# Kernel optimization log

Hardware: AMD Instinct MI355X
Metric: run time of the kernel (lower is better)

## Reference

```python
import jax, jax.numpy as jnp
import numpy as np

EPS = 1e-8

def _batch_gather(table, idx):
    # table: (B, M, F), idx: (B, K) -> (B, K, F)
    return jnp.take_along_axis(table, idx[:, :, None], axis=1)

def setup_inputs() -> dict:
    key = jax.random.key(0)
    ks = jax.random.split(key, 8)
    B, N, E, K, F = 8, 4096, 16384, 16, 128
    initial_node_embed = jax.random.normal(ks[0], (B, N, F), dtype=jnp.float32)
    edges = jax.random.randint(ks[1], (B, E, 3), 0, N, dtype=jnp.int64)
    node_edges = jax.random.randint(ks[2], (B, N, K), 0, E, dtype=jnp.int64)
    node_edge_mask = jax.random.randint(ks[3], (B, N, K), 0, 2, dtype=jnp.int32)
    s = 1.0 / np.sqrt(F)
    W1 = jax.random.normal(ks[4], (F, F), dtype=jnp.float32) * s
    b1 = jnp.zeros((F,), dtype=jnp.float32)
    W2 = jax.random.normal(ks[5], (F, F), dtype=jnp.float32) * s
    b2 = jnp.zeros((F,), dtype=jnp.float32)
    return {"initial_node_embed": initial_node_embed, "edges": edges,
            "node_edges": node_edges, "node_edge_mask": node_edge_mask,
            "W1": W1, "b1": b1, "W2": W2, "b2": b2}

def reference(initial_node_embed, edges, node_edges, node_edge_mask, W1, b1, W2, b2):
    B, N, F = initial_node_embed.shape
    K = node_edges.shape[2]
    sender_idx = edges[:, :, 0]                      # (B, E)
    mask_f = node_edge_mask.astype(jnp.float32)      # (B, N, K)
    num_neighbors = jnp.sum(mask_f, 2, keepdims=True) + EPS  # (B, N, 1)
    flat_ne = node_edges.reshape(B, -1)              # (B, N*K)

    def mp(node_emb, W, b):
        sender = _batch_gather(node_emb, sender_idx)             # (B, E, F)
        edge_emb = jnp.tanh(sender @ W.T + b)                    # (B, E, F)
        nbr = _batch_gather(edge_emb, flat_ne).reshape(B, N, K, F)
        nbr = nbr * mask_f[:, :, :, None]
        return jnp.sum(nbr, 2) / num_neighbors                   # avg agg

    x0 = initial_node_embed
    x1 = mp(x0, W1, b1)
    x2 = mp(x1, W2, b2)
    return jnp.concatenate([x0, x1, x2], axis=2)     # (B, N, 3F)
```

## Files before the change

kernel.cpp:

```cpp
#include <hip/hip_runtime.h>
#include <hip/hip_bf16.h>

typedef __attribute__((ext_vector_type(8))) short short8;
typedef __attribute__((ext_vector_type(4))) float f32x4;
typedef __attribute__((ext_vector_type(2))) float f32x2;

#define B_ 8
#define N_ 4096
#define E_ 16384
#define K_ 16
#define F_ 128

#if defined(__has_builtin)
#  if __has_builtin(__builtin_amdgcn_cvt_pk_f32_fp8) && __has_builtin(__builtin_amdgcn_cvt_pk_fp8_f32)
#    define HW_FP8 1
#  endif
#endif

__device__ __forceinline__ unsigned short f2bf(float f) {
    union { float f; unsigned int u; } c; c.f = f;
    unsigned int u = c.u;
    unsigned int r = (u + 0x7fffu + ((u >> 16) & 1u)) >> 16;
    return (unsigned short)r;
}
__device__ __forceinline__ float fast_tanh(float x) {
    float e = __expf(2.0f * x);
    return 1.0f - 2.0f / (e + 1.0f);
}

__device__ __forceinline__ unsigned int f2fp8_manual(float v) {
    unsigned int u = __float_as_uint(v * 0x1p-120f);
    unsigned int r = (u & 0x7fffffffu) + 0x7ffffu + ((u >> 20) & 1u);
    return ((r >> 20) & 0x7fu) | ((u >> 24) & 0x80u);
}
__device__ __forceinline__ unsigned int pack_fp8x4(float t0, float t1, float t2, float t3) {
#ifdef HW_FP8
    int wd = 0;
    wd = __builtin_amdgcn_cvt_pk_fp8_f32(t0, t1, wd, false);
    wd = __builtin_amdgcn_cvt_pk_fp8_f32(t2, t3, wd, true);
    return (unsigned int)wd;
#else
    return f2fp8_manual(t0) | (f2fp8_manual(t1) << 8) |
           (f2fp8_manual(t2) << 16) | (f2fp8_manual(t3) << 24);
#endif
}
#ifndef HW_FP8
#define DECM(bb) __int_as_float((int)((((bb) & 0x80u) << 24) | (((bb) & 0x7fu) << 20)))
#endif

__device__ __forceinline__ int detect64(const int* raw) {
    int o = 0;
    #pragma unroll
    for (int i = 1; i < 128; i += 2) o |= raw[i];
    return (o == 0) ? 1 : 0;
}

__global__ void wprep(const float* __restrict__ W1, const float* __restrict__ W2,
                      const int* __restrict__ edges_raw, const int* __restrict__ ne_raw,
                      unsigned short* __restrict__ wf, int* __restrict__ flags) {
    int blk = blockIdx.x, tid = threadIdx.x;
    if (blk == 16) {
        if (tid == 0) {
            flags[0] = detect64(edges_raw);
            flags[1] = detect64(ne_raw);
        }
        return;
    }
    int gtid = blk * 256 + tid;
    int wsel = gtid >> 11;
    int q = gtid & 2047;
    int lane = q & 63;
    int gq = q >> 6;
    int nt = gq >> 2, g = gq & 3;
    const float* W = wsel ? W2 : W1;
    int j = nt * 16 + (lane & 15);
    int kbase = g * 32 + 8 * (lane >> 4);
    unsigned short* d = wf + wsel * 16384 + q * 8;
    #pragma unroll
    for (int t = 0; t < 8; ++t) d[t] = f2bf(W[j * 128 + kbase + t]);
}

__global__ void __launch_bounds__(256) node_kernel(
    const float* __restrict__ xsrc, const int* __restrict__ edges_raw,
    const int* __restrict__ ne_raw, const int* __restrict__ mask,
    const int* __restrict__ flags, const unsigned short* __restrict__ wf,
    const float* __restrict__ bias, unsigned char* __restrict__ y,
    float* __restrict__ out, int* __restrict__ sid2) {
    __shared__ short xt[64 * F_];
    int tid = threadIdx.x;
    int swz = (blockIdx.x & 7) * 64 + (blockIdx.x >> 3);
    int b = swz >> 6;
    int r0 = (swz & 63) * 64;
    {
        int s64e = flags[0], s64n = flags[1];
        int base = swz * 1024;
        #pragma unroll
        for (int t = 0; t < 4; ++t) {
            int i = base + t * 256 + tid;
            int bb = i >> 16;
            int eid = s64n ? ne_raw[2 * (long long)i] : ne_raw[i];
            long long ei = (long long)(bb * E_ + eid);
            int s = s64e ? edges_raw[6 * ei] : edges_raw[3 * ei];
            sid2[i] = mask[i] ? s : -1;
        }
    }
    #pragma unroll
    for (int c = 0; c < 4; ++c) {
        int ci = tid + 256 * c;
        int row = ci >> 4, ch = ci & 15;
        int pch = ch ^ (row & 15);
        long long gnode = (long long)(b * N_ + r0 + row);
        const float* src = xsrc + gnode * F_ + ch * 8;
        float4 v0 = *(const float4*)src;
        float4 v1 = *(const float4*)(src + 4);
        ushort4 h0, h1;
        h0.x = f2bf(v0.x); h0.y = f2bf(v0.y); h0.z = f2bf(v0.z); h0.w = f2bf(v0.w);
        h1.x = f2bf(v1.x); h1.y = f2bf(v1.y); h1.z = f2bf(v1.z); h1.w = f2bf(v1.w);
        *(ushort4*)&xt[row * F_ + pch * 8] = h0;
        *(ushort4*)&xt[row * F_ + pch * 8 + 4] = h1;
        float* od = out + gnode * 384 + ch * 8;
        *(float4*)od = v0;
        *(float4*)(od + 4) = v1;
    }
    __syncthreads();
    int w = tid >> 6, lane = tid & 63;
    int rr = w * 16 + (lane & 15);
    short8 bfr[4];
    #pragma unroll
    for (int g = 0; g < 4; ++g) {
        int pch = (g * 4 + (lane >> 4)) ^ (rr & 15);
        bfr[g] = *(const short8*)&xt[rr * F_ + pch * 8];
    }
    int jq = (lane >> 4) * 4;
    long long ybyte = ((long long)(b * N_ + r0 + w * 16 + (lane & 15))) * F_;
    #pragma unroll
    for (int nt = 0; nt < 8; ++nt) {
        f32x4 acc = (f32x4){0.f, 0.f, 0.f, 0.f};
        #pragma unroll
        for (int g = 0; g < 4; ++g) {
            short8 afr = *(const short8*)(wf + ((nt * 4 + g) * 64 + lane) * 8);
            acc = __builtin_amdgcn_mfma_f32_16x16x32_bf16(afr, bfr[g], acc, 0, 0, 0);
        }
        float4 bv = *(const float4*)(bias + nt * 16 + jq);
        float t0 = fast_tanh(acc[0] + bv.x);
        float t1 = fast_tanh(acc[1] + bv.y);
        float t2 = fast_tanh(acc[2] + bv.z);
        float t3 = fast_tanh(acc[3] + bv.w);
        *(unsigned int*)(y + ybyte + nt * 16 + jq) = pack_fp8x4(t0, t1, t2, t3);
    }
}

__global__ void __launch_bounds__(256) aggnode_kernel(
    const unsigned char* __restrict__ y1, const int* __restrict__ sid2,
    const unsigned short* __restrict__ wf2, const float* __restrict__ bias,
    float* __restrict__ out, unsigned char* __restrict__ y2) {
    __shared__ short xt[64 * F_];
    int tid = threadIdx.x;
    int swz = (blockIdx.x & 7) * 64 + (blockIdx.x >> 3);
    int b = swz >> 6;
    int r0 = (swz & 63) * 64;
    int wid = tid >> 6, lane = tid & 63;
    int qt = lane >> 4, s16 = lane & 15;
    const unsigned char* ybase = y1 + (long long)b * (N_ * F_) + s16 * 8;
    #pragma unroll
    for (int t = 0; t < 4; ++t) {
        int row = wid * 16 + qt * 4 + t;
        long long gnode = (long long)(b * N_ + r0 + row);
        const int4* ip = (const int4*)(sid2 + gnode * K_);
        int4 i0 = ip[0], i1 = ip[1], i2 = ip[2], i3 = ip[3];
        float cnt = (float)((i0.x >= 0) + (i0.y >= 0) + (i0.z >= 0) + (i0.w >= 0) +
                            (i1.x >= 0) + (i1.y >= 0) + (i1.z >= 0) + (i1.w >= 0) +
                            (i2.x >= 0) + (i2.y >= 0) + (i2.z >= 0) + (i2.w >= 0) +
                            (i3.x >= 0) + (i3.y >= 0) + (i3.z >= 0) + (i3.w >= 0));
        float a0 = 0.f, a1 = 0.f, a2 = 0.f, a3 = 0.f;
        float a4 = 0.f, a5 = 0.f, a6 = 0.f, a7 = 0.f;
#ifdef HW_FP8
        #define PROC(pk) { \
            float m = ((pk) >= 0) ? 1.0f : 0.0f; \
            int nid = (pk) < 0 ? 0 : (pk); \
            uint2 v = *(const uint2*)(ybase + (long long)nid * F_); \
            f32x2 c0 = __builtin_amdgcn_cvt_pk_f32_fp8(v.x, false); \
            f32x2 c1 = __builtin_amdgcn_cvt_pk_f32_fp8(v.x, true); \
            f32x2 c2 = __builtin_amdgcn_cvt_pk_f32_fp8(v.y, false); \
            f32x2 c3 = __builtin_amdgcn_cvt_pk_f32_fp8(v.y, true); \
            a0 += m * c0.x; a1 += m * c0.y; a2 += m * c1.x; a3 += m * c1.y; \
            a4 += m * c2.x; a5 += m * c2.y; a6 += m * c3.x; a7 += m * c3.y; }
#else
        #define PROC(pk) { \
            float ms = ((pk) >= 0) ? 0x1p120f : 0.0f; \
            int nid = (pk) < 0 ? 0 : (pk); \
            uint2 v = *(const uint2*)(ybase + (long long)nid * F_); \
            a0 += ms * DECM(v.x); a1 += ms * DECM(v.x >> 8); \
            a2 += ms * DECM(v.x >> 16); a3 += ms * DECM(v.x >> 24); \
            a4 += ms * DECM(v.y); a5 += ms * DECM(v.y >> 8); \
            a6 += ms * DECM(v.y >> 16); a7 += ms * DECM(v.y >> 24); }
#endif
        PROC(i0.x) PROC(i0.y) PROC(i0.z) PROC(i0.w)
        PROC(i1.x) PROC(i1.y) PROC(i1.z) PROC(i1.w)
        PROC(i2.x) PROC(i2.y) PROC(i2.z) PROC(i2.w)
        PROC(i3.x) PROC(i3.y) PROC(i3.z) PROC(i3.w)
        #undef PROC
        float inv = 1.0f / (cnt + 1e-8f);
        a0 *= inv; a1 *= inv; a2 *= inv; a3 *= inv;
        a4 *= inv; a5 *= inv; a6 *= inv; a7 *= inv;
        float* po = out + gnode * 384 + 128 + s16 * 8;
        *(f32x4*)po = (f32x4){a0, a1, a2, a3};
        *(f32x4*)(po + 4) = (f32x4){a4, a5, a6, a7};
        int pch = s16 ^ (row & 15);
        short8 h;
        h[0] = (short)f2bf(a0); h[1] = (short)f2bf(a1);
        h[2] = (short)f2bf(a2); h[3] = (short)f2bf(a3);
        h[4] = (short)f2bf(a4); h[5] = (short)f2bf(a5);
        h[6] = (short)f2bf(a6); h[7] = (short)f2bf(a7);
        *(short8*)&xt[row * F_ + pch * 8] = h;
    }
    __syncthreads();
    int rr = wid * 16 + (lane & 15);
    short8 bfr[4];
    #pragma unroll
    for (int g = 0; g < 4; ++g) {
        int pch = (g * 4 + (lane >> 4)) ^ (rr & 15);
        bfr[g] = *(const short8*)&xt[rr * F_ + pch * 8];
    }
    int jq = (lane >> 4) * 4;
    long long ybyte = ((long long)(b * N_ + r0 + wid * 16 + (lane & 15))) * F_;
    #pragma unroll
    for (int nt = 0; nt < 8; ++nt) {
        f32x4 acc = (f32x4){0.f, 0.f, 0.f, 0.f};
        #pragma unroll
        for (int g = 0; g < 4; ++g) {
            short8 afr = *(const short8*)(wf2 + ((nt * 4 + g) * 64 + lane) * 8);
            acc = __builtin_amdgcn_mfma_f32_16x16x32_bf16(afr, bfr[g], acc, 0, 0, 0);
        }
        float4 bv = *(const float4*)(bias + nt * 16 + jq);
        float t0 = fast_tanh(acc[0] + bv.x);
        float t1 = fast_tanh(acc[1] + bv.y);
        float t2 = fast_tanh(acc[2] + bv.z);
        float t3 = fast_tanh(acc[3] + bv.w);
        *(unsigned int*)(y2 + ybyte + nt * 16 + jq) = pack_fp8x4(t0, t1, t2, t3);
    }
}

__global__ void __launch_bounds__(256) agg_kernel(
    const unsigned char* __restrict__ y, const int* __restrict__ sid2,
    float* __restrict__ out, int col_off) {
    int tid = threadIdx.x;
    int swz = (blockIdx.x & 7) * 256 + (blockIdx.x >> 3);
    int nodeblk = swz * 16;
    int wid = tid >> 6, lane = tid & 63;
    int qt = lane >> 4, s16 = lane & 15;
    int node = nodeblk + wid * 4 + qt;
    int b = node >> 12;
    const int4* ip = (const int4*)(sid2 + node * K_);
    int4 i0 = ip[0], i1 = ip[1], i2 = ip[2], i3 = ip[3];
    float cnt = (float)((i0.x >= 0) + (i0.y >= 0) + (i0.z >= 0) + (i0.w >= 0) +
                        (i1.x >= 0) + (i1.y >= 0) + (i1.z >= 0) + (i1.w >= 0) +
                        (i2.x >= 0) + (i2.y >= 0) + (i2.z >= 0) + (i2.w >= 0) +
                        (i3.x >= 0) + (i3.y >= 0) + (i3.z >= 0) + (i3.w >= 0));
    const unsigned char* ybase = y + (long long)b * (N_ * F_) + s16 * 8;
    float a0 = 0.f, a1 = 0.f, a2 = 0.f, a3 = 0.f;
    float a4 = 0.f, a5 = 0.f, a6 = 0.f, a7 = 0.f;
#ifdef HW_FP8
    #define PROC(pk) { \
        float m = ((pk) >= 0) ? 1.0f : 0.0f; \
        int nid = (pk) < 0 ? 0 : (pk); \
        uint2 v = *(const uint2*)(ybase + (long long)nid * F_); \
        f32x2 c0 = __builtin_amdgcn_cvt_pk_f32_fp8(v.x, false); \
        f32x2 c1 = __builtin_amdgcn_cvt_pk_f32_fp8(v.x, true); \
        f32x2 c2 = __builtin_amdgcn_cvt_pk_f32_fp8(v.y, false); \
        f32x2 c3 = __builtin_amdgcn_cvt_pk_f32_fp8(v.y, true); \
        a0 += m * c0.x; a1 += m * c0.y; a2 += m * c1.x; a3 += m * c1.y; \
        a4 += m * c2.x; a5 += m * c2.y; a6 += m * c3.x; a7 += m * c3.y; }
#else
    #define PROC(pk) { \
        float ms = ((pk) >= 0) ? 0x1p120f : 0.0f; \
        int nid = (pk) < 0 ? 0 : (pk); \
        uint2 v = *(const uint2*)(ybase + (long long)nid * F_); \
        a0 += ms * DECM(v.x); a1 += ms * DECM(v.x >> 8); \
        a2 += ms * DECM(v.x >> 16); a3 += ms * DECM(v.x >> 24); \
        a4 += ms * DECM(v.y); a5 += ms * DECM(v.y >> 8); \
        a6 += ms * DECM(v.y >> 16); a7 += ms * DECM(v.y >> 24); }
#endif
    PROC(i0.x) PROC(i0.y) PROC(i0.z) PROC(i0.w)
    PROC(i1.x) PROC(i1.y) PROC(i1.z) PROC(i1.w)
    PROC(i2.x) PROC(i2.y) PROC(i2.z) PROC(i2.w)
    PROC(i3.x) PROC(i3.y) PROC(i3.z) PROC(i3.w)
    #undef PROC
    float inv = 1.0f / (cnt + 1e-8f);
    a0 *= inv; a1 *= inv; a2 *= inv; a3 *= inv;
    a4 *= inv; a5 *= inv; a6 *= inv; a7 *= inv;
    float* po = out + (long long)node * 384 + col_off + s16 * 8;
    *(f32x4*)po = (f32x4){a0, a1, a2, a3};
    *(f32x4*)(po + 4) = (f32x4){a4, a5, a6, a7};
}

extern "C" void kernel_launch(void* const* d_in, const int* in_sizes, int n_in,
                              void* d_out, int out_size, void* d_ws, size_t ws_size,
                              hipStream_t stream) {
    const float* x0        = (const float*)d_in[0];
    const int*   edges_raw = (const int*)d_in[1];
    const int*   ne_raw    = (const int*)d_in[2];
    const int*   mask      = (const int*)d_in[3];
    const float* W1        = (const float*)d_in[4];
    const float* b1        = (const float*)d_in[5];
    const float* W2        = (const float*)d_in[6];
    const float* b2        = (const float*)d_in[7];
    float* out = (float*)d_out;
    char* ws = (char*)d_ws;

    unsigned char*  y1   = (unsigned char*)ws;
    unsigned char*  y2   = (unsigned char*)(ws + 4194304);
    unsigned short* wf   = (unsigned short*)(ws + 8388608);
    int* flags           = (int*)(ws + 8454144);
    int* sid2            = (int*)(ws + 8519680);

    wprep<<<17, 256, 0, stream>>>(W1, W2, edges_raw, ne_raw, wf, flags);
    node_kernel<<<512, 256, 0, stream>>>(x0, edges_raw, ne_raw, mask,
                                         flags, wf, b1, y1, out, sid2);
    aggnode_kernel<<<512, 256, 0, stream>>>(y1, sid2, wf + 16384, b2, out, y2);
    agg_kernel<<<2048, 256, 0, stream>>>(y2, sid2, out, 256);
}
```

Measured before the change: 46.88 us.

## Fuse three stage kernels into one persistent kernel with per-batch atomic barriers

Merges the node transform, the first aggregation plus second transform, and the final aggregation into a single kernel of 512 blocks. Stages are separated by per-batch group barriers that spin on atomic counters in global memory, 64 blocks per batch. This removes two kernel launches and the tail and drain gaps between them. The barrier relies on every block of a group being co-resident on the GPU, uses relaxed atomics with no explicit memory fence, and adds spin-wait overhead.

```diff
diff --git a/kernel.cpp b/kernel.cpp
--- a/kernel.cpp
+++ b/kernel.cpp
@@ -64,6 +64,7 @@
             flags[0] = detect64(edges_raw);
             flags[1] = detect64(ne_raw);
         }
+        if (tid < 16) flags[4 + tid] = 0;
         return;
     }
     int gtid = blk * 256 + tid;
@@ -80,17 +81,34 @@
     for (int t = 0; t < 8; ++t) d[t] = f2bf(W[j * 128 + kbase + t]);
 }
 
-__global__ void __launch_bounds__(256) node_kernel(
-    const float* __restrict__ xsrc, const int* __restrict__ edges_raw,
+__device__ __forceinline__ void group_bar(int* c) {
+    __syncthreads();
+    if (threadIdx.x == 0) {
+        __hip_atomic_fetch_add(c, 1, __ATOMIC_RELAXED, __HIP_MEMORY_SCOPE_AGENT);
+        while (__hip_atomic_load(c, __ATOMIC_RELAXED, __HIP_MEMORY_SCOPE_AGENT) < 64) {
+            __builtin_amdgcn_s_sleep(2);
+        }
+    }
+    __syncthreads();
+}
+
+__global__ void __launch_bounds__(256) mega_kernel(
+    const float* __restrict__ x0, const int* __restrict__ edges_raw,
     const int* __restrict__ ne_raw, const int* __restrict__ mask,
-    const int* __restrict__ flags, const unsigned short* __restrict__ wf,
-    const float* __restrict__ bias, unsigned char* __restrict__ y,
-    float* __restrict__ out, int* __restrict__ sid2) {
+    int* __restrict__ flags, const unsigned short* __restrict__ wf,
+    const float* __restrict__ b1, const float* __restrict__ b2,
+    unsigned char* __restrict__ y1, unsigned char* __restrict__ y2,
+    int* __restrict__ sid2, float* __restrict__ out) {
     __shared__ short xt[64 * F_];
     int tid = threadIdx.x;
-    int swz = (blockIdx.x & 7) * 64 + (blockIdx.x >> 3);
+    int blk = blockIdx.x;
+    int grp = blk & 7;
+    int swz = grp * 64 + (blk >> 3);
     int b = swz >> 6;
     int r0 = (swz & 63) * 64;
+    int wid = tid >> 6, lane = tid & 63;
+    int qt = lane >> 4, s16 = lane & 15;
+
     {
         int s64e = flags[0], s64n = flags[1];
         int base = swz * 1024;
@@ -110,7 +128,7 @@
         int row = ci >> 4, ch = ci & 15;
         int pch = ch ^ (row & 15);
         long long gnode = (long long)(b * N_ + r0 + row);
-        const float* src = xsrc + gnode * F_ + ch * 8;
+        const float* src = x0 + gnode * F_ + ch * 8;
         float4 v0 = *(const float4*)src;
         float4 v1 = *(const float4*)(src + 4);
         ushort4 h0, h1;
@@ -123,175 +141,164 @@
         *(float4*)(od + 4) = v1;
     }
     __syncthreads();
-    int w = tid >> 6, lane = tid & 63;
-    int rr = w * 16 + (lane & 15);
-    short8 bfr[4];
-    #pragma unroll
-    for (int g = 0; g < 4; ++g) {
-        int pch = (g * 4 + (lane >> 4)) ^ (rr & 15);
-        bfr[g] = *(const short8*)&xt[rr * F_ + pch * 8];
-    }
-    int jq = (lane >> 4) * 4;
-    long long ybyte = ((long long)(b * N_ + r0 + w * 16 + (lane & 15))) * F_;
-    #pragma unroll
-    for (int nt = 0; nt < 8; ++nt) {
-        f32x4 acc = (f32x4){0.f, 0.f, 0.f, 0.f};
+    {
+        int rr = wid * 16 + (lane & 15);
+        short8 bfr[4];
         #pragma unroll
         for (int g = 0; g < 4; ++g) {
-            short8 afr = *(const short8*)(wf + ((nt * 4 + g) * 64 + lane) * 8);
-            acc = __builtin_amdgcn_mfma_f32_16x16x32_bf16(afr, bfr[g], acc, 0, 0, 0);
-        }
-        float4 bv = *(const float4*)(bias + nt * 16 + jq);
-        float t0 = fast_tanh(acc[0] + bv.x);
-        float t1 = fast_tanh(acc[1] + bv.y);
-        float t2 = fast_tanh(acc[2] + bv.z);
-        float t3 = fast_tanh(acc[3] + bv.w);
-        *(unsigned int*)(y + ybyte + nt * 16 + jq) = pack_fp8x4(t0, t1, t2, t3);
-    }
-}
-
-__global__ void __launch_bounds__(256) aggnode_kernel(
-    const unsigned char* __restrict__ y1, const int* __restrict__ sid2,
-    const unsigned short* __restrict__ wf2, const float* __restrict__ bias,
-    float* __restrict__ out, unsigned char* __restrict__ y2) {
-    __shared__ short xt[64 * F_];
-    int tid = threadIdx.x;
-    int swz = (blockIdx.x & 7) * 64 + (blockIdx.x >> 3);
-    int b = swz >> 6;
-    int r0 = (swz & 63) * 64;
-    int wid = tid >> 6, lane = tid & 63;
-    int qt = lane >> 4, s16 = lane & 15;
-    const unsigned char* ybase = y1 + (long long)b * (N_ * F_) + s16 * 8;
-    #pragma unroll
-    for (int t = 0; t < 4; ++t) {
-        int row = wid * 16 + qt * 4 + t;
-        long long gnode = (long long)(b * N_ + r0 + row);
-        const int4* ip = (const int4*)(sid2 + gnode * K_);
-        int4 i0 = ip[0], i1 = ip[1], i2 = ip[2], i3 = ip[3];
-        float cnt = (float)((i0.x >= 0) + (i0.y >= 0) + (i0.z >= 0) + (i0.w >= 0) +
-                            (i1.x >= 0) + (i1.y >= 0) + (i1.z >= 0) + (i1.w >= 0) +
-                            (i2.x >= 0) + (i2.y >= 0) + (i2.z >= 0) + (i2.w >= 0) +
-                            (i3.x >= 0) + (i3.y >= 0) + (i3.z >= 0) + (i3.w >= 0));
-        float a0 = 0.f, a1 = 0.f, a2 = 0.f, a3 = 0.f;
-        float a4 = 0.f, a5 = 0.f, a6 = 0.f, a7 = 0.f;
+            int pch = (g * 4 + (lane >> 4)) ^ (rr & 15);
+            bfr[g] = *(const short8*)&xt[rr * F_ + pch * 8];
+        }
+        int jq = (lane >> 4) * 4;
+        long long ybyte = ((long long)(b * N_ + r0 + wid * 16 + (lane & 15))) * F_;
+        #pragma unroll
+        for (int nt = 0; nt < 8; ++nt) {
+            f32x4 acc = (f32x4){0.f, 0.f, 0.f, 0.f};
+            #pragma unroll
+            for (int g = 0; g < 4; ++g) {
+                short8 afr = *(const short8*)(wf + ((nt * 4 + g) * 64 + lane) * 8);
+                acc = __builtin_amdgcn_mfma_f32_16x16x32_bf16(afr, bfr[g], acc, 0, 0, 0);
+            }
+            float4 bv = *(const float4*)(b1 + nt * 16 + jq);
+            float t0 = fast_tanh(acc[0] + bv.x);
+            float t1 = fast_tanh(acc[1] + bv.y);
+            float t2 = fast_tanh(acc[2] + bv.z);
+            float t3 = fast_tanh(acc[3] + bv.w);
+            *(unsigned int*)(y1 + ybyte + nt * 16 + jq) = pack_fp8x4(t0, t1, t2, t3);
+        }
+    }
+    group_bar(flags + 4 + grp);
+
+    {
+        const unsigned char* ybase = y1 + (long long)b * (N_ * F_) + s16 * 8;
+        #pragma unroll
+        for (int t = 0; t < 4; ++t) {
+            int row = wid * 16 + qt * 4 + t;
+            long long gnode = (long long)(b * N_ + r0 + row);
+            const int4* ip = (const int4*)(sid2 + gnode * K_);
+            int4 i0 = ip[0], i1 = ip[1], i2 = ip[2], i3 = ip[3];
+            float cnt = (float)((i0.x >= 0) + (i0.y >= 0) + (i0.z >= 0) + (i0.w >= 0) +
+                                (i1.x >= 0) + (i1.y >= 0) + (i1.z >= 0) + (i1.w >= 0) +
+                                (i2.x >= 0) + (i2.y >= 0) + (i2.z >= 0) + (i2.w >= 0) +
+                                (i3.x >= 0) + (i3.y >= 0) + (i3.z >= 0) + (i3.w >= 0));
+            float a0 = 0.f, a1 = 0.f, a2 = 0.f, a3 = 0.f;
+            float a4 = 0.f, a5 = 0.f, a6 = 0.f, a7 = 0.f;
 #ifdef HW_FP8
-        #define PROC(pk) { \
-            float m = ((pk) >= 0) ? 1.0f : 0.0f; \
-            int nid = (pk) < 0 ? 0 : (pk); \
-            uint2 v = *(const uint2*)(ybase + (long long)nid * F_); \
-            f32x2 c0 = __builtin_amdgcn_cvt_pk_f32_fp8(v.x, false); \
-            f32x2 c1 = __builtin_amdgcn_cvt_pk_f32_fp8(v.x, true); \
-            f32x2 c2 = __builtin_amdgcn_cvt_pk_f32_fp8(v.y, false); \
-            f32x2 c3 = __builtin_amdgcn_cvt_pk_f32_fp8(v.y, true); \
-            a0 += m * c0.x; a1 += m * c0.y; a2 += m * c1.x; a3 += m * c1.y; \
-            a4 += m * c2.x; a5 += m * c2.y; a6 += m * c3.x; a7 += m * c3.y; }
+            #define PROC(pk) { \
+                float m = ((pk) >= 0) ? 1.0f : 0.0f; \
+                int nid = (pk) < 0 ? 0 : (pk); \
+                uint2 v = *(const uint2*)(ybase + (long long)nid * F_); \
+                f32x2 c0 = __builtin_amdgcn_cvt_pk_f32_fp8(v.x, false); \
+                f32x2 c1 = __builtin_amdgcn_cvt_pk_f32_fp8(v.x, true); \
+                f32x2 c2 = __builtin_amdgcn_cvt_pk_f32_fp8(v.y, false); \
+                f32x2 c3 = __builtin_amdgcn_cvt_pk_f32_fp8(v.y, true); \
+                a0 += m * c0.x; a1 += m * c0.y; a2 += m * c1.x; a3 += m * c1.y; \
+                a4 += m * c2.x; a5 += m * c2.y; a6 += m * c3.x; a7 += m * c3.y; }
 #else
-        #define PROC(pk) { \
-            float ms = ((pk) >= 0) ? 0x1p120f : 0.0f; \
-            int nid = (pk) < 0 ? 0 : (pk); \
-            uint2 v = *(const uint2*)(ybase + (long long)nid * F_); \
-            a0 += ms * DECM(v.x); a1 += ms * DECM(v.x >> 8); \
-            a2 += ms * DECM(v.x >> 16); a3 += ms * DECM(v.x >> 24); \
-            a4 += ms * DECM(v.y); a5 += ms * DECM(v.y >> 8); \
-            a6 += ms * DECM(v.y >> 16); a7 += ms * DECM(v.y >> 24); }
-#endif
-        PROC(i0.x) PROC(i0.y) PROC(i0.z) PROC(i0.w)
-        PROC(i1.x) PROC(i1.y) PROC(i1.z) PROC(i1.w)
-        PROC(i2.x) PROC(i2.y) PROC(i2.z) PROC(i2.w)
-        PROC(i3.x) PROC(i3.y) PROC(i3.z) PROC(i3.w)
-        #undef PROC
-        float inv = 1.0f / (cnt + 1e-8f);
-        a0 *= inv; a1 *= inv; a2 *= inv; a3 *= inv;
-        a4 *= inv; a5 *= inv; a6 *= inv; a7 *= inv;
-        float* po = out + gnode * 384 + 128 + s16 * 8;
-        *(f32x4*)po = (f32x4){a0, a1, a2, a3};
-        *(f32x4*)(po + 4) = (f32x4){a4, a5, a6, a7};
-        int pch = s16 ^ (row & 15);
-        short8 h;
-        h[0] = (short)f2bf(a0); h[1] = (short)f2bf(a1);
-        h[2] = (short)f2bf(a2); h[3] = (short)f2bf(a3);
-        h[4] = (short)f2bf(a4); h[5] = (short)f2bf(a5);
-        h[6] = (short)f2bf(a6); h[7] = (short)f2bf(a7);
-        *(short8*)&xt[row * F_ + pch * 8] = h;
-    }
-    __syncthreads();
-    int rr = wid * 16 + (lane & 15);
-    short8 bfr[4];
-    #pragma unroll
-    for (int g = 0; g < 4; ++g) {
-        int pch = (g * 4 + (lane >> 4)) ^ (rr & 15);
-        bfr[g] = *(const short8*)&xt[rr * F_ + pch * 8];
-    }
-    int jq = (lane >> 4) * 4;
-    long long ybyte = ((long long)(b * N_ + r0 + wid * 16 + (lane & 15))) * F_;
-    #pragma unroll
-    for (int nt = 0; nt < 8; ++nt) {
-        f32x4 acc = (f32x4){0.f, 0.f, 0.f, 0.f};
+            #define PROC(pk) { \
+                float ms = ((pk) >= 0) ? 0x1p120f : 0.0f; \
+                int nid = (pk) < 0 ? 0 : (pk); \
+                uint2 v = *(const uint2*)(ybase + (long long)nid * F_); \
+                a0 += ms * DECM(v.x); a1 += ms * DECM(v.x >> 8); \
+                a2 += ms * DECM(v.x >> 16); a3 += ms * DECM(v.x >> 24); \
+                a4 += ms * DECM(v.y); a5 += ms * DECM(v.y >> 8); \
+                a6 += ms * DECM(v.y >> 16); a7 += ms * DECM(v.y >> 24); }
+#endif
+            PROC(i0.x) PROC(i0.y) PROC(i0.z) PROC(i0.w)
+            PROC(i1.x) PROC(i1.y) PROC(i1.z) PROC(i1.w)
+            PROC(i2.x) PROC(i2.y) PROC(i2.z) PROC(i2.w)
+            PROC(i3.x) PROC(i3.y) PROC(i3.z) PROC(i3.w)
+            #undef PROC
+            float inv = 1.0f / (cnt + 1e-8f);
+            a0 *= inv; a1 *= inv; a2 *= inv; a3 *= inv;
+            a4 *= inv; a5 *= inv; a6 *= inv; a7 *= inv;
+            float* po = out + gnode * 384 + 128 + s16 * 8;
+            *(f32x4*)po = (f32x4){a0, a1, a2, a3};
+            *(f32x4*)(po + 4) = (f32x4){a4, a5, a6, a7};
+            int pch = s16 ^ (row & 15);
+            short8 h;
+            h[0] = (short)f2bf(a0); h[1] = (short)f2bf(a1);
+            h[2] = (short)f2bf(a2); h[3] = (short)f2bf(a3);
+            h[4] = (short)f2bf(a4); h[5] = (short)f2bf(a5);
+            h[6] = (short)f2bf(a6); h[7] = (short)f2bf(a7);
+            *(short8*)&xt[row * F_ + pch * 8] = h;
+        }
+        __syncthreads();
+        int rr = wid * 16 + (lane & 15);
+        short8 bfr[4];
         #pragma unroll
         for (int g = 0; g < 4; ++g) {
-            short8 afr = *(const short8*)(wf2 + ((nt * 4 + g) * 64 + lane) * 8);
-            acc = __builtin_amdgcn_mfma_f32_16x16x32_bf16(afr, bfr[g], acc, 0, 0, 0);
-        }
-        float4 bv = *(const float4*)(bias + nt * 16 + jq);
-        float t0 = fast_tanh(acc[0] + bv.x);
-        float t1 = fast_tanh(acc[1] + bv.y);
-        float t2 = fast_tanh(acc[2] + bv.z);
-        float t3 = fast_tanh(acc[3] + bv.w);
-        *(unsigned int*)(y2 + ybyte + nt * 16 + jq) = pack_fp8x4(t0, t1, t2, t3);
-    }
-}
-
-__global__ void __launch_bounds__(256) agg_kernel(
-    const unsigned char* __restrict__ y, const int* __restrict__ sid2,
-    float* __restrict__ out, int col_off) {
-    int tid = threadIdx.x;
-    int swz = (blockIdx.x & 7) * 256 + (blockIdx.x >> 3);
-    int nodeblk = swz * 16;
-    int wid = tid >> 6, lane = tid & 63;
-    int qt = lane >> 4, s16 = lane & 15;
-    int node = nodeblk + wid * 4 + qt;
-    int b = node >> 12;
-    const int4* ip = (const int4*)(sid2 + node * K_);
-    int4 i0 = ip[0], i1 = ip[1], i2 = ip[2], i3 = ip[3];
-    float cnt = (float)((i0.x >= 0) + (i0.y >= 0) + (i0.z >= 0) + (i0.w >= 0) +
-                        (i1.x >= 0) + (i1.y >= 0) + (i1.z >= 0) + (i1.w >= 0) +
-                        (i2.x >= 0) + (i2.y >= 0) + (i2.z >= 0) + (i2.w >= 0) +
-                        (i3.x >= 0) + (i3.y >= 0) + (i3.z >= 0) + (i3.w >= 0));
-    const unsigned char* ybase = y + (long long)b * (N_ * F_) + s16 * 8;
-    float a0 = 0.f, a1 = 0.f, a2 = 0.f, a3 = 0.f;
-    float a4 = 0.f, a5 = 0.f, a6 = 0.f, a7 = 0.f;
+            int pch = (g * 4 + (lane >> 4)) ^ (rr & 15);
+            bfr[g] = *(const short8*)&xt[rr * F_ + pch * 8];
+        }
+        int jq = (lane >> 4) * 4;
+        long long ybyte = ((long long)(b * N_ + r0 + wid * 16 + (lane & 15))) * F_;
+        #pragma unroll
+        for (int nt = 0; nt < 8; ++nt) {
+            f32x4 acc = (f32x4){0.f, 0.f, 0.f, 0.f};
+            #pragma unroll
+            for (int g = 0; g < 4; ++g) {
+                short8 afr = *(const short8*)(wf + 16384 + ((nt * 4 + g) * 64 + lane) * 8);
+                acc = __builtin_amdgcn_mfma_f32_16x16x32_bf16(afr, bfr[g], acc, 0, 0, 0);
+            }
+            float4 bv = *(const float4*)(b2 + nt * 16 + jq);
+            float t0 = fast_tanh(acc[0] + bv.x);
+            float t1 = fast_tanh(acc[1] + bv.y);
+            float t2 = fast_tanh(acc[2] + bv.z);
+            float t3 = fast_tanh(acc[3] + bv.w);
+            *(unsigned int*)(y2 + ybyte + nt * 16 + jq) = pack_fp8x4(t0, t1, t2, t3);
+        }
+    }
+    group_bar(flags + 12 + grp);
+
+    {
+        const unsigned char* ybase = y2 + (long long)b * (N_ * F_) + s16 * 8;
+        #pragma unroll
+        for (int t = 0; t < 4; ++t) {
+            int row = wid * 16 + qt * 4 + t;
+            long long gnode = (long long)(b * N_ + r0 + row);
+            const int4* ip = (const int4*)(sid2 + gnode * K_);
+            int4 i0 = ip[0], i1 = ip[1], i2 = ip[2], i3 = ip[3];
+            float cnt = (float)((i0.x >= 0) + (i0.y >= 0) + (i0.z >= 0) + (i0.w >= 0) +
+                                (i1.x >= 0) + (i1.y >= 0) + (i1.z >= 0) + (i1.w >= 0) +
+                                (i2.x >= 0) + (i2.y >= 0) + (i2.z >= 0) + (i2.w >= 0) +
+                                (i3.x >= 0) + (i3.y >= 0) + (i3.z >= 0) + (i3.w >= 0));
+            float a0 = 0.f, a1 = 0.f, a2 = 0.f, a3 = 0.f;
+            float a4 = 0.f, a5 = 0.f, a6 = 0.f, a7 = 0.f;
 #ifdef HW_FP8
-    #define PROC(pk) { \
-        float m = ((pk) >= 0) ? 1.0f : 0.0f; \
-        int nid = (pk) < 0 ? 0 : (pk); \
-        uint2 v = *(const uint2*)(ybase + (long long)nid * F_); \
-        f32x2 c0 = __builtin_amdgcn_cvt_pk_f32_fp8(v.x, false); \
-        f32x2 c1 = __builtin_amdgcn_cvt_pk_f32_fp8(v.x, true); \
-        f32x2 c2 = __builtin_amdgcn_cvt_pk_f32_fp8(v.y, false); \
-        f32x2 c3 = __builtin_amdgcn_cvt_pk_f32_fp8(v.y, true); \
-        a0 += m * c0.x; a1 += m * c0.y; a2 += m * c1.x; a3 += m * c1.y; \
-        a4 += m * c2.x; a5 += m * c2.y; a6 += m * c3.x; a7 += m * c3.y; }
+            #define PROC(pk) { \
+                float m = ((pk) >= 0) ? 1.0f : 0.0f; \
+                int nid = (pk) < 0 ? 0 : (pk); \
+                uint2 v = *(const uint2*)(ybase + (long long)nid * F_); \
+                f32x2 c0 = __builtin_amdgcn_cvt_pk_f32_fp8(v.x, false); \
+                f32x2 c1 = __builtin_amdgcn_cvt_pk_f32_fp8(v.x, true); \
+                f32x2 c2 = __builtin_amdgcn_cvt_pk_f32_fp8(v.y, false); \
+                f32x2 c3 = __builtin_amdgcn_cvt_pk_f32_fp8(v.y, true); \
+                a0 += m * c0.x; a1 += m * c0.y; a2 += m * c1.x; a3 += m * c1.y; \
+                a4 += m * c2.x; a5 += m * c2.y; a6 += m * c3.x; a7 += m * c3.y; }
 #else
-    #define PROC(pk) { \
-        float ms = ((pk) >= 0) ? 0x1p120f : 0.0f; \
-        int nid = (pk) < 0 ? 0 : (pk); \
-        uint2 v = *(const uint2*)(ybase + (long long)nid * F_); \
-        a0 += ms * DECM(v.x); a1 += ms * DECM(v.x >> 8); \
-        a2 += ms * DECM(v.x >> 16); a3 += ms * DECM(v.x >> 24); \
-        a4 += ms * DECM(v.y); a5 += ms * DECM(v.y >> 8); \
-        a6 += ms * DECM(v.y >> 16); a7 += ms * DECM(v.y >> 24); }
-#endif
-    PROC(i0.x) PROC(i0.y) PROC(i0.z) PROC(i0.w)
-    PROC(i1.x) PROC(i1.y) PROC(i1.z) PROC(i1.w)
-    PROC(i2.x) PROC(i2.y) PROC(i2.z) PROC(i2.w)
-    PROC(i3.x) PROC(i3.y) PROC(i3.z) PROC(i3.w)
-    #undef PROC
-    float inv = 1.0f / (cnt + 1e-8f);
-    a0 *= inv; a1 *= inv; a2 *= inv; a3 *= inv;
-    a4 *= inv; a5 *= inv; a6 *= inv; a7 *= inv;
-    float* po = out + (long long)node * 384 + col_off + s16 * 8;
-    *(f32x4*)po = (f32x4){a0, a1, a2, a3};
-    *(f32x4*)(po + 4) = (f32x4){a4, a5, a6, a7};
+            #define PROC(pk) { \
+                float ms = ((pk) >= 0) ? 0x1p120f : 0.0f; \
+                int nid = (pk) < 0 ? 0 : (pk); \
+                uint2 v = *(const uint2*)(ybase + (long long)nid * F_); \
+                a0 += ms * DECM(v.x); a1 += ms * DECM(v.x >> 8); \
+                a2 += ms * DECM(v.x >> 16); a3 += ms * DECM(v.x >> 24); \
+                a4 += ms * DECM(v.y); a5 += ms * DECM(v.y >> 8); \
+                a6 += ms * DECM(v.y >> 16); a7 += ms * DECM(v.y >> 24); }
+#endif
+            PROC(i0.x) PROC(i0.y) PROC(i0.z) PROC(i0.w)
+            PROC(i1.x) PROC(i1.y) PROC(i1.z) PROC(i1.w)
+            PROC(i2.x) PROC(i2.y) PROC(i2.z) PROC(i2.w)
+            PROC(i3.x) PROC(i3.y) PROC(i3.z) PROC(i3.w)
+            #undef PROC
+            float inv = 1.0f / (cnt + 1e-8f);
+            a0 *= inv; a1 *= inv; a2 *= inv; a3 *= inv;
+            a4 *= inv; a5 *= inv; a6 *= inv; a7 *= inv;
+            float* po = out + gnode * 384 + 256 + s16 * 8;
+            *(f32x4*)po = (f32x4){a0, a1, a2, a3};
+            *(f32x4*)(po + 4) = (f32x4){a4, a5, a6, a7};
+        }
+    }
 }
 
 extern "C" void kernel_launch(void* const* d_in, const int* in_sizes, int n_in,
@@ -315,8 +322,6 @@
     int* sid2            = (int*)(ws + 8519680);
 
     wprep<<<17, 256, 0, stream>>>(W1, W2, edges_raw, ne_raw, wf, flags);
-    node_kernel<<<512, 256, 0, stream>>>(x0, edges_raw, ne_raw, mask,
-                                         flags, wf, b1, y1, out, sid2);
-    aggnode_kernel<<<512, 256, 0, stream>>>(y1, sid2, wf + 16384, b2, out, y2);
-    agg_kernel<<<2048, 256, 0, stream>>>(y2, sid2, out, 256);
-}
+    mega_kernel<<<512, 256, 0, stream>>>(x0, edges_raw, ne_raw, mask, flags,
+                                         wf, b1, b2, y1, y2, sid2, out);
+}
```

Result: slower. 67.39 us (+43.7%).
